# Performance work log

Measured on AMD Instinct MI355X. Metric: run time of the kernel, lower is better.

## Reference

```python
import jax, jax.numpy as jnp
import numpy as np

NEG_INF = -1e30  # stand-in for float('-inf') that is softmax-safe


def setup_inputs() -> dict:
    key = jax.random.key(0)
    ks = jax.random.split(key, 6)
    B, H, S, D = 2, 8, 1024, 64
    NF, K = 4, 3
    return {
        "query": jax.random.normal(ks[0], (B, H, S, D), dtype=jnp.float32),
        "keys": jax.random.normal(ks[1], (B, H, S, D), dtype=jnp.float32),
        "vals": jax.random.normal(ks[2], (B, H, S, D), dtype=jnp.float32),
        "mask": jnp.ones((B, 1, S, S), dtype=jnp.int32),
        "conv_w": jax.random.normal(ks[3], (NF, 1, K, K), dtype=jnp.float32) * (1.0 / K),
        "conv_b": jnp.zeros((NF,), dtype=jnp.float32),
        "lin_w": jax.random.normal(ks[4], (1, NF), dtype=jnp.float32) * 0.5,
        "lin_b": jnp.zeros((1,), dtype=jnp.float32),
    }


def reference(query, keys, vals, mask, conv_w, conv_b, lin_w, lin_b):
    B, H, S, D = query.shape
    NF = conv_w.shape[0]
    K = conv_w.shape[2]
    scale = jnp.asarray(D, query.dtype) ** 0.5

    # [B,H,S,S] raw dot-product scores
    dp = jnp.einsum("bhsd,bhtd->bhst", query, keys) / scale

    # conv2d over the score matrix: treat (B*H) as batch, 1 input channel
    x = dp.reshape(B * H, 1, S, S)
    conv = jax.lax.conv_general_dilated(
        x, conv_w,
        window_strides=(1, 1),
        padding=[(K // 2, K // 2), (K // 2, K // 2)],
        dimension_numbers=("NCHW", "OIHW", "NCHW"),
    ) + conv_b[None, :, None, None]
    conv = jax.nn.leaky_relu(conv, negative_slope=0.01)  # [B*H, NF, S, S]

    # per-pixel linear over the filter axis (Linear(num_filters, 1))
    conv = conv.reshape(B, H, NF, S, S)
    preattn = jnp.einsum("bhfst,f->bhst", conv, lin_w[0]) + lin_b[0]

    # masking + softmax (mask broadcasts over heads)
    preattn = jnp.where(mask == 0, jnp.asarray(NEG_INF, preattn.dtype), preattn)
    attn = jax.nn.softmax(preattn, axis=-1)

    # dropout is identity in eval mode
    return jnp.einsum("bhst,bhtd->bhsd", attn, vals)
```

## Files before the change

### kernel.cpp

```cpp
#include <hip/hip_runtime.h>
#include <math.h>

#define S_LEN 1024
#define D_DIM 64
#define NBH   16

typedef unsigned short ushort_t;
typedef __attribute__((ext_vector_type(8))) short short8;
typedef __attribute__((ext_vector_type(4))) short short4v;
typedef __attribute__((ext_vector_type(4))) float f32x4;
typedef __attribute__((ext_vector_type(2))) float f32x2;

__device__ __forceinline__ ushort_t rne_bf16(float x) {
    unsigned u = __float_as_uint(x);
    return (ushort_t)((u + 0x7FFFu + ((u >> 16) & 1u)) >> 16);
}
__device__ __forceinline__ void split1(float x, ushort_t& h, ushort_t& l) {
    h = rne_bf16(x);
    float hf = __uint_as_float((unsigned)h << 16);
    l = rne_bf16(x - hf);
}

__global__ __launch_bounds__(256) void prep(
    const float* __restrict__ k, const float* __restrict__ v,
    const int* __restrict__ mask,
    ushort_t* __restrict__ khi, ushort_t* __restrict__ klo,
    ushort_t* __restrict__ vhi, ushort_t* __restrict__ vlo,
    unsigned* __restrict__ mw)
{
    __shared__ float Ls[64][65];
    const int tid = threadIdx.x;
    const int bx = blockIdx.x;
    if (bx < 512) {
        const int gid  = bx * 256 + tid;
        const int bh   = gid >> 13;
        const int tile = (gid >> 7) & 63;
        const int ch   = (gid >> 6) & 1;
        const int lane = gid & 63;
        const int quad = lane >> 4, t15 = lane & 15;
        const float* src = k + ((size_t)bh * S_LEN + tile * 16 + t15) * D_DIM
                             + ch * 32 + quad * 8;
        float x[8];
        *(float4*)(x + 0) = *(const float4*)(src);
        *(float4*)(x + 4) = *(const float4*)(src + 4);
        short8 hv, lv;
        #pragma unroll
        for (int i = 0; i < 8; ++i) {
            ushort_t h, l;
            split1(x[i], h, l);
            hv[i] = (short)h; lv[i] = (short)l;
        }
        *(short8*)(khi + (size_t)gid * 8) = hv;
        *(short8*)(klo + (size_t)gid * 8) = lv;
    } else if (bx < 768) {
        const int bi = bx - 512;
        const int tt = bi & 15, bh = bi >> 4;
        const float* vb = v + ((size_t)bh * S_LEN + tt * 64) * D_DIM;
        #pragma unroll
        for (int p = 0; p < 4; ++p) {
            int idx = p * 1024 + tid * 4;
            int r = idx >> 6, c = idx & 63;
            float4 x = *(const float4*)(vb + r * 64 + c);
            Ls[r][c] = x.x; Ls[r][c+1] = x.y; Ls[r][c+2] = x.z; Ls[r][c+3] = x.w;
        }
        __syncthreads();
        const int d = tid >> 2, c0 = (tid & 3) * 16;
        ushort_t hi[16], lo[16];
        #pragma unroll
        for (int j = 0; j < 16; ++j) split1(Ls[c0 + j][d], hi[j], lo[j]);
        const int tb0 = tt * 8 + (c0 >> 3);
        const size_t o0 = (((size_t)bh * 128 + tb0) * 64 + d) * 8;
        const size_t o1 = (((size_t)bh * 128 + tb0 + 1) * 64 + d) * 8;
        *(short8*)(vhi + o0) = *(short8*)(hi);
        *(short8*)(vhi + o1) = *(short8*)(hi + 8);
        *(short8*)(vlo + o0) = *(short8*)(lo);
        *(short8*)(vlo + o1) = *(short8*)(lo + 8);
    } else {
        const int gid = (bx - 768) * 256 + tid;
        const int row = gid >> 5, wd = gid & 31;
        const int4* mp = (const int4*)(mask + (size_t)row * 1024 + wd * 32);
        unsigned bits = 0;
        #pragma unroll
        for (int p = 0; p < 8; ++p) {
            int4 qv = mp[p];
            bits |= (qv.x != 0 ? 1u : 0u) << (p * 4 + 0);
            bits |= (qv.y != 0 ? 1u : 0u) << (p * 4 + 1);
            bits |= (qv.z != 0 ? 1u : 0u) << (p * 4 + 2);
            bits |= (qv.w != 0 ? 1u : 0u) << (p * 4 + 3);
        }
        mw[(size_t)row * 32 + wd] = bits;
    }
}

__global__ __launch_bounds__(256) void qk_mfma(
    const float* __restrict__ q,
    const ushort_t* __restrict__ khi, const ushort_t* __restrict__ klo,
    float* __restrict__ dp)
{
    __shared__ float Ls[4][16][68];
    const int st = blockIdx.x, bh = blockIdx.y;
    const int s0 = st * 16;
    const int tid = threadIdx.x;
    const int wave = tid >> 6, lane = tid & 63;
    const int m = lane & 15, quad = lane >> 4;

    const float* qp = q + ((size_t)bh * S_LEN + s0 + m) * D_DIM + quad * 8;
    float qa[16];
    *(float4*)(qa + 0)  = *(const float4*)(qp + 0);
    *(float4*)(qa + 4)  = *(const float4*)(qp + 4);
    *(float4*)(qa + 8)  = *(const float4*)(qp + 32);
    *(float4*)(qa + 12) = *(const float4*)(qp + 36);
    short8 ahi0, alo0, ahi1, alo1;
    #pragma unroll
    for (int i = 0; i < 8; ++i) {
        ushort_t h, l;
        split1(qa[i], h, l);      ahi0[i] = (short)h; alo0[i] = (short)l;
        split1(qa[8 + i], h, l);  ahi1[i] = (short)h; alo1[i] = (short)l;
    }

    float* dpb = dp + ((size_t)bh * S_LEN + s0) * S_LEN;

    #pragma unroll
    for (int sub = 0; sub < 4; ++sub) {
        #pragma unroll
        for (int tt = 0; tt < 4; ++tt) {
            const int tile = wave * 16 + sub * 4 + tt;
            const size_t kb = (((size_t)bh * 64 + tile) * 128 + lane) * 8;
            short8 bhi0 = *(const short8*)(khi + kb);
            short8 blo0 = *(const short8*)(klo + kb);
            short8 bhi1 = *(const short8*)(khi + kb + 512);
            short8 blo1 = *(const short8*)(klo + kb + 512);
            f32x4 acc = {0.f, 0.f, 0.f, 0.f};
            acc = __builtin_amdgcn_mfma_f32_16x16x32_bf16(ahi0, bhi0, acc, 0, 0, 0);
            acc = __builtin_amdgcn_mfma_f32_16x16x32_bf16(ahi0, blo0, acc, 0, 0, 0);
            acc = __builtin_amdgcn_mfma_f32_16x16x32_bf16(alo0, bhi0, acc, 0, 0, 0);
            acc = __builtin_amdgcn_mfma_f32_16x16x32_bf16(ahi1, bhi1, acc, 0, 0, 0);
            acc = __builtin_amdgcn_mfma_f32_16x16x32_bf16(ahi1, blo1, acc, 0, 0, 0);
            acc = __builtin_amdgcn_mfma_f32_16x16x32_bf16(alo1, bhi1, acc, 0, 0, 0);
            #pragma unroll
            for (int r = 0; r < 4; ++r)
                Ls[wave][quad * 4 + r][tt * 16 + m] = acc[r] * 0.125f;
        }
        const int cb = wave * 256 + sub * 64;
        #pragma unroll
        for (int p = 0; p < 4; ++p) {
            const int row = p * 4 + (lane >> 4);
            const int f4  = lane & 15;
            float4 val = *(const float4*)&Ls[wave][row][f4 * 4];
            *(float4*)&dpb[(size_t)row * S_LEN + cb + f4 * 4] = val;
        }
    }
}

#define PSTR 1048
__global__ __launch_bounds__(512) void conv_av(
    const float* __restrict__ dp, const unsigned* __restrict__ mw,
    const ushort_t* __restrict__ vhi, const ushort_t* __restrict__ vlo,
    const float* __restrict__ conv_w, const float* __restrict__ conv_b,
    const float* __restrict__ lin_w, const float* __restrict__ lin_b,
    float* __restrict__ out)
{
    __shared__ ushort_t pP[16 * PSTR];
    __shared__ float oBuf[16][68];
    __shared__ float lsPart[16][4];
    __shared__ unsigned mb[16][32];

    const int st = blockIdx.x, bh = blockIdx.y;
    const int s0 = st * 16;
    const int b  = bh >> 3;
    const int tid = threadIdx.x;
    const int wave = tid >> 6, lane = tid & 63;
    const int m = lane & 15, quad = lane >> 4;

    {
        const int row = tid >> 5, wd = tid & 31;
        mb[row][wd] = mw[((size_t)b * S_LEN + s0 + row) * 32 + wd];
    }

    float w[36];
    #pragma unroll
    for (int i = 0; i < 36; ++i) w[i] = conv_w[i];
    float cb[4], lw[4];
    #pragma unroll
    for (int f = 0; f < 4; ++f) { cb[f] = conv_b[f]; lw[f] = lin_w[f]; }
    const float lb = lin_b[0];

    const int rh = tid >> 8, cg = tid & 255, c0 = cg * 4;
    const float* dpb = dp + (size_t)bh * S_LEN * S_LEN;
    __syncthreads();

    #pragma unroll
    for (int pass = 0; pass < 2; ++pass) {
        const int obase = rh * 8 + pass * 4;
        float rowv[6][6];
        #pragma unroll
        for (int jj = 0; jj < 6; ++jj) {
            const int ir = s0 + obase - 1 + jj;
            if (ir >= 0 && ir < S_LEN) {
                const float* rp = dpb + (size_t)ir * S_LEN + c0;
                f32x4 md = *(const f32x4*)rp;
                rowv[jj][0] = cg ? rp[-1] : 0.f;
                rowv[jj][1] = md.x; rowv[jj][2] = md.y;
                rowv[jj][3] = md.z; rowv[jj][4] = md.w;
                rowv[jj][5] = (cg < 255) ? rp[4] : 0.f;
            } else {
                #pragma unroll
                for (int i = 0; i < 6; ++i) rowv[jj][i] = 0.f;
            }
        }
        float ls[4];
        #pragma unroll
        for (int jo = 0; jo < 4; ++jo) {
            const int o = obase + jo;
            f32x2 pa = {lb, lb}, pb = {lb, lb};
            #pragma unroll
            for (int f = 0; f < 4; ++f) {
                f32x2 ca = {cb[f], cb[f]}, cbv = ca;
                #pragma unroll
                for (int dr = 0; dr < 3; ++dr) {
                    const float* vv = rowv[jo + dr];
                    #pragma unroll
                    for (int dc = 0; dc < 3; ++dc) {
                        const float wt = w[f * 9 + dr * 3 + dc];
                        f32x2 ia = {vv[dc],     vv[dc + 1]};
                        f32x2 ib = {vv[dc + 2], vv[dc + 3]};
                        ca  += wt * ia;
                        cbv += wt * ib;
                    }
                }
                f32x2 la  = {fmaxf(ca.x, 0.f)  + 0.01f * fminf(ca.x, 0.f),
                             fmaxf(ca.y, 0.f)  + 0.01f * fminf(ca.y, 0.f)};
                f32x2 lb2 = {fmaxf(cbv.x, 0.f) + 0.01f * fminf(cbv.x, 0.f),
                             fmaxf(cbv.y, 0.f) + 0.01f * fminf(cbv.y, 0.f)};
                pa += lw[f] * la;
                pb += lw[f] * lb2;
            }
            const unsigned word = mb[o][cg >> 3];
            const unsigned nib  = (word >> ((cg & 7) * 4)) & 0xFu;
            float pre[4] = {pa.x, pa.y, pb.x, pb.y};
            #pragma unroll
            for (int i = 0; i < 4; ++i)
                if (!((nib >> i) & 1u)) pre[i] = -1e30f;
            float pv[4];
            #pragma unroll
            for (int i = 0; i < 4; ++i) pv[i] = __expf(pre[i]);
            ls[jo] = (pv[0] + pv[1]) + (pv[2] + pv[3]);
            short4v hv = {(short)rne_bf16(pv[0]), (short)rne_bf16(pv[1]),
                          (short)rne_bf16(pv[2]), (short)rne_bf16(pv[3])};
            *(short4v*)&pP[o * PSTR + c0] = hv;
        }
        #pragma unroll
        for (int jo = 0; jo < 4; ++jo) {
            float t = ls[jo];
            #pragma unroll
            for (int off = 1; off < 64; off <<= 1) t += __shfl_xor(t, off);
            if (lane == 0) lsPart[obase + jo][wave & 3] = t;
        }
    }
    __syncthreads();

    const int d0 = (wave & 3) * 16;
    const int th = wave >> 2;
    f32x4 O = {0.f, 0.f, 0.f, 0.f};
    #pragma unroll 4
    for (int i = 0; i < 16; ++i) {
        const int c = th * 16 + i;
        short8 ph = *(const short8*)&pP[m * PSTR + c * 32 + quad * 8];
        const size_t vb = (((size_t)bh * 128 + c * 4 + quad) * 64 + d0 + m) * 8;
        short8 vh = *(const short8*)(vhi + vb);
        short8 vl = *(const short8*)(vlo + vb);
        O = __builtin_amdgcn_mfma_f32_16x16x32_bf16(ph, vh, O, 0, 0, 0);
        O = __builtin_amdgcn_mfma_f32_16x16x32_bf16(ph, vl, O, 0, 0, 0);
    }
    if (wave < 4) {
        #pragma unroll
        for (int r = 0; r < 4; ++r) oBuf[quad * 4 + r][d0 + m] = O[r];
    }
    __syncthreads();
    if (wave >= 4) {
        #pragma unroll
        for (int r = 0; r < 4; ++r) {
            const int br = quad * 4 + r;
            const float lsum = (lsPart[br][0] + lsPart[br][1]) +
                               (lsPart[br][2] + lsPart[br][3]);
            out[((size_t)bh * S_LEN + s0 + br) * D_DIM + d0 + m] =
                (O[r] + oBuf[br][d0 + m]) / lsum;
        }
    }
}

extern "C" void kernel_launch(void* const* d_in, const int* in_sizes, int n_in,
                              void* d_out, int out_size, void* d_ws, size_t ws_size,
                              hipStream_t stream) {
    const float* q      = (const float*)d_in[0];
    const float* k      = (const float*)d_in[1];
    const float* v      = (const float*)d_in[2];
    const int*   mask   = (const int*)d_in[3];
    const float* conv_w = (const float*)d_in[4];
    const float* conv_b = (const float*)d_in[5];
    const float* lin_w  = (const float*)d_in[6];
    const float* lin_b  = (const float*)d_in[7];
    float* out = (float*)d_out;

    char* wsb = (char*)d_ws;
    const size_t MB = 1024 * 1024;
    ushort_t* khi = (ushort_t*)(wsb + 0 * MB);
    ushort_t* klo = (ushort_t*)(wsb + 2 * MB);
    ushort_t* vhi = (ushort_t*)(wsb + 4 * MB);
    ushort_t* vlo = (ushort_t*)(wsb + 6 * MB);
    unsigned* mw  = (unsigned*)(wsb + 8 * MB);
    float*    dp  = (float*)(wsb + 16 * MB);

    prep<<<dim3(1024), 256, 0, stream>>>(k, v, mask, khi, klo, vhi, vlo, mw);
    qk_mfma<<<dim3(64, NBH), 256, 0, stream>>>(q, khi, klo, dp);
    conv_av<<<dim3(64, NBH), 512, 0, stream>>>(
        dp, mw, vhi, vlo, conv_w, conv_b, lin_w, lin_b, out);
}
```

Baseline: 136.2 us.

## Fuse QK score computation into conv/AV kernel with fp16 LDS halo tile

Removes the separate qk_mfma kernel and the 64 MB fp32 score matrix round-trip through global memory. Each block now computes its 16 score rows plus a one-row halo on each side directly with MFMA and stores them as fp16 in shared memory for the 3x3 conv stage. The cost is recomputing halo rows, extra MFMA work for the second 16-row set, more LDS per block (which may lower occupancy), and fp16 rounding of the scores before the conv.

Result: faster. 131.8 us (-3.2%).

```diff
diff --git a/kernel.cpp b/kernel.cpp
--- a/kernel.cpp
+++ b/kernel.cpp
@@ -6,10 +6,12 @@
 #define NBH   16
 
 typedef unsigned short ushort_t;
+typedef unsigned int uint_t;
 typedef __attribute__((ext_vector_type(8))) short short8;
 typedef __attribute__((ext_vector_type(4))) short short4v;
 typedef __attribute__((ext_vector_type(4))) float f32x4;
 typedef __attribute__((ext_vector_type(2))) float f32x2;
+typedef __attribute__((ext_vector_type(2))) _Float16 h2;
 
 __device__ __forceinline__ ushort_t rne_bf16(float x) {
     unsigned u = __float_as_uint(x);
@@ -19,6 +21,22 @@
     h = rne_bf16(x);
     float hf = __uint_as_float((unsigned)h << 16);
     l = rne_bf16(x - hf);
+}
+__device__ __forceinline__ ushort_t f16bits(float x) {
+    _Float16 h = (_Float16)x;
+    ushort_t b;
+    __builtin_memcpy(&b, &h, 2);
+    return b;
+}
+__device__ __forceinline__ float h2f(ushort_t b) {
+    _Float16 h;
+    __builtin_memcpy(&h, &b, 2);
+    return (float)h;
+}
+__device__ __forceinline__ h2 as_h2(uint_t u) {
+    h2 r;
+    __builtin_memcpy(&r, &u, 4);
+    return r;
 }
 
 __global__ __launch_bounds__(256) void prep(
@@ -92,74 +110,18 @@
     }
 }
 
-__global__ __launch_bounds__(256) void qk_mfma(
+#define DPSTR 1040
+#define PSTR  1048
+__global__ __launch_bounds__(512) void fused_qk_conv_av(
     const float* __restrict__ q,
     const ushort_t* __restrict__ khi, const ushort_t* __restrict__ klo,
-    float* __restrict__ dp)
-{
-    __shared__ float Ls[4][16][68];
-    const int st = blockIdx.x, bh = blockIdx.y;
-    const int s0 = st * 16;
-    const int tid = threadIdx.x;
-    const int wave = tid >> 6, lane = tid & 63;
-    const int m = lane & 15, quad = lane >> 4;
-
-    const float* qp = q + ((size_t)bh * S_LEN + s0 + m) * D_DIM + quad * 8;
-    float qa[16];
-    *(float4*)(qa + 0)  = *(const float4*)(qp + 0);
-    *(float4*)(qa + 4)  = *(const float4*)(qp + 4);
-    *(float4*)(qa + 8)  = *(const float4*)(qp + 32);
-    *(float4*)(qa + 12) = *(const float4*)(qp + 36);
-    short8 ahi0, alo0, ahi1, alo1;
-    #pragma unroll
-    for (int i = 0; i < 8; ++i) {
-        ushort_t h, l;
-        split1(qa[i], h, l);      ahi0[i] = (short)h; alo0[i] = (short)l;
-        split1(qa[8 + i], h, l);  ahi1[i] = (short)h; alo1[i] = (short)l;
-    }
-
-    float* dpb = dp + ((size_t)bh * S_LEN + s0) * S_LEN;
-
-    #pragma unroll
-    for (int sub = 0; sub < 4; ++sub) {
-        #pragma unroll
-        for (int tt = 0; tt < 4; ++tt) {
-            const int tile = wave * 16 + sub * 4 + tt;
-            const size_t kb = (((size_t)bh * 64 + tile) * 128 + lane) * 8;
-            short8 bhi0 = *(const short8*)(khi + kb);
-            short8 blo0 = *(const short8*)(klo + kb);
-            short8 bhi1 = *(const short8*)(khi + kb + 512);
-            short8 blo1 = *(const short8*)(klo + kb + 512);
-            f32x4 acc = {0.f, 0.f, 0.f, 0.f};
-            acc = __builtin_amdgcn_mfma_f32_16x16x32_bf16(ahi0, bhi0, acc, 0, 0, 0);
-            acc = __builtin_amdgcn_mfma_f32_16x16x32_bf16(ahi0, blo0, acc, 0, 0, 0);
-            acc = __builtin_amdgcn_mfma_f32_16x16x32_bf16(alo0, bhi0, acc, 0, 0, 0);
-            acc = __builtin_amdgcn_mfma_f32_16x16x32_bf16(ahi1, bhi1, acc, 0, 0, 0);
-            acc = __builtin_amdgcn_mfma_f32_16x16x32_bf16(ahi1, blo1, acc, 0, 0, 0);
-            acc = __builtin_amdgcn_mfma_f32_16x16x32_bf16(alo1, bhi1, acc, 0, 0, 0);
-            #pragma unroll
-            for (int r = 0; r < 4; ++r)
-                Ls[wave][quad * 4 + r][tt * 16 + m] = acc[r] * 0.125f;
-        }
-        const int cb = wave * 256 + sub * 64;
-        #pragma unroll
-        for (int p = 0; p < 4; ++p) {
-            const int row = p * 4 + (lane >> 4);
-            const int f4  = lane & 15;
-            float4 val = *(const float4*)&Ls[wave][row][f4 * 4];
-            *(float4*)&dpb[(size_t)row * S_LEN + cb + f4 * 4] = val;
-        }
-    }
-}
-
-#define PSTR 1048
-__global__ __launch_bounds__(512) void conv_av(
-    const float* __restrict__ dp, const unsigned* __restrict__ mw,
+    const unsigned* __restrict__ mw,
     const ushort_t* __restrict__ vhi, const ushort_t* __restrict__ vlo,
     const float* __restrict__ conv_w, const float* __restrict__ conv_b,
     const float* __restrict__ lin_w, const float* __restrict__ lin_b,
     float* __restrict__ out)
 {
+    __shared__ ushort_t dpH[18 * DPSTR];
     __shared__ ushort_t pP[16 * PSTR];
     __shared__ float oBuf[16][68];
     __shared__ float lsPart[16][4];
@@ -177,6 +139,72 @@
         mb[row][wd] = mw[((size_t)b * S_LEN + s0 + row) * 32 + wd];
     }
 
+    short8 AH0[2], AH1[2], AL0[2], AL1[2];
+    #pragma unroll
+    for (int set = 0; set < 2; ++set) {
+        const int sA = s0 - 1 + 2 * set + m;
+        const int sQ = sA < 0 ? 0 : (sA > S_LEN - 1 ? S_LEN - 1 : sA);
+        const float* qp = q + ((size_t)bh * S_LEN + sQ) * D_DIM + quad * 8;
+        float qa[16];
+        *(float4*)(qa + 0)  = *(const float4*)(qp + 0);
+        *(float4*)(qa + 4)  = *(const float4*)(qp + 4);
+        *(float4*)(qa + 8)  = *(const float4*)(qp + 32);
+        *(float4*)(qa + 12) = *(const float4*)(qp + 36);
+        #pragma unroll
+        for (int i = 0; i < 8; ++i) {
+            ushort_t h, l;
+            split1(qa[i] * 0.125f, h, l);
+            AH0[set][i] = (short)h; AL0[set][i] = (short)l;
+            split1(qa[8 + i] * 0.125f, h, l);
+            AH1[set][i] = (short)h; AL1[set][i] = (short)l;
+        }
+    }
+
+    #pragma unroll
+    for (int tt = 0; tt < 8; ++tt) {
+        const int tile = wave * 8 + tt;
+        const size_t kb = (((size_t)bh * 64 + tile) * 128 + lane) * 8;
+        short8 KH0 = *(const short8*)(khi + kb);
+        short8 KL0 = *(const short8*)(klo + kb);
+        short8 KH1 = *(const short8*)(khi + kb + 512);
+        short8 KL1 = *(const short8*)(klo + kb + 512);
+        const int col = tile * 16 + m;
+        {
+            f32x4 a0 = {0.f, 0.f, 0.f, 0.f}, a1 = {0.f, 0.f, 0.f, 0.f};
+            a0 = __builtin_amdgcn_mfma_f32_16x16x32_bf16(AH0[0], KH0, a0, 0, 0, 0);
+            a1 = __builtin_amdgcn_mfma_f32_16x16x32_bf16(AH1[0], KH1, a1, 0, 0, 0);
+            a0 = __builtin_amdgcn_mfma_f32_16x16x32_bf16(AH0[0], KL0, a0, 0, 0, 0);
+            a1 = __builtin_amdgcn_mfma_f32_16x16x32_bf16(AH1[0], KL1, a1, 0, 0, 0);
+            a0 = __builtin_amdgcn_mfma_f32_16x16x32_bf16(AL0[0], KH0, a0, 0, 0, 0);
+            a1 = __builtin_amdgcn_mfma_f32_16x16x32_bf16(AL1[0], KH1, a1, 0, 0, 0);
+            #pragma unroll
+            for (int r = 0; r < 4; ++r) {
+                const int row = quad * 4 + r;
+                const int s = s0 - 1 + row;
+                const float v = (s >= 0 && s < S_LEN) ? a0[r] + a1[r] : 0.f;
+                dpH[row * DPSTR + col] = f16bits(v);
+            }
+        }
+        {
+            f32x4 a0 = {0.f, 0.f, 0.f, 0.f}, a1 = {0.f, 0.f, 0.f, 0.f};
+            a0 = __builtin_amdgcn_mfma_f32_16x16x32_bf16(AH0[1], KH0, a0, 0, 0, 0);
+            a1 = __builtin_amdgcn_mfma_f32_16x16x32_bf16(AH1[1], KH1, a1, 0, 0, 0);
+            a0 = __builtin_amdgcn_mfma_f32_16x16x32_bf16(AH0[1], KL0, a0, 0, 0, 0);
+            a1 = __builtin_amdgcn_mfma_f32_16x16x32_bf16(AH1[1], KL1, a1, 0, 0, 0);
+            a0 = __builtin_amdgcn_mfma_f32_16x16x32_bf16(AL0[1], KH0, a0, 0, 0, 0);
+            a1 = __builtin_amdgcn_mfma_f32_16x16x32_bf16(AL1[1], KH1, a1, 0, 0, 0);
+            if (quad == 3) {
+                #pragma unroll
+                for (int r = 2; r < 4; ++r) {
+                    const int mrow = quad * 4 + r;
+                    const int s = s0 + 1 + mrow;
+                    const float v = (s < S_LEN) ? a0[r] + a1[r] : 0.f;
+                    dpH[(mrow + 2) * DPSTR + col] = f16bits(v);
+                }
+            }
+        }
+    }
+
     float w[36];
     #pragma unroll
     for (int i = 0; i < 36; ++i) w[i] = conv_w[i];
@@ -185,28 +213,22 @@
     for (int f = 0; f < 4; ++f) { cb[f] = conv_b[f]; lw[f] = lin_w[f]; }
     const float lb = lin_b[0];
 
+    __syncthreads();
+
     const int rh = tid >> 8, cg = tid & 255, c0 = cg * 4;
-    const float* dpb = dp + (size_t)bh * S_LEN * S_LEN;
-    __syncthreads();
-
     #pragma unroll
     for (int pass = 0; pass < 2; ++pass) {
         const int obase = rh * 8 + pass * 4;
         float rowv[6][6];
         #pragma unroll
         for (int jj = 0; jj < 6; ++jj) {
-            const int ir = s0 + obase - 1 + jj;
-            if (ir >= 0 && ir < S_LEN) {
-                const float* rp = dpb + (size_t)ir * S_LEN + c0;
-                f32x4 md = *(const f32x4*)rp;
-                rowv[jj][0] = cg ? rp[-1] : 0.f;
-                rowv[jj][1] = md.x; rowv[jj][2] = md.y;
-                rowv[jj][3] = md.z; rowv[jj][4] = md.w;
-                rowv[jj][5] = (cg < 255) ? rp[4] : 0.f;
-            } else {
-                #pragma unroll
-                for (int i = 0; i < 6; ++i) rowv[jj][i] = 0.f;
-            }
+            const ushort_t* rp = &dpH[(obase + jj) * DPSTR + c0];
+            uint2 dd = *(const uint2*)rp;
+            h2 p0 = as_h2(dd.x), p1 = as_h2(dd.y);
+            rowv[jj][0] = cg ? h2f(rp[-1]) : 0.f;
+            rowv[jj][1] = (float)p0[0]; rowv[jj][2] = (float)p0[1];
+            rowv[jj][3] = (float)p1[0]; rowv[jj][4] = (float)p1[1];
+            rowv[jj][5] = (cg < 255) ? h2f(rp[4]) : 0.f;
         }
         float ls[4];
         #pragma unroll
@@ -309,10 +331,8 @@
     ushort_t* vhi = (ushort_t*)(wsb + 4 * MB);
     ushort_t* vlo = (ushort_t*)(wsb + 6 * MB);
     unsigned* mw  = (unsigned*)(wsb + 8 * MB);
-    float*    dp  = (float*)(wsb + 16 * MB);
 
     prep<<<dim3(1024), 256, 0, stream>>>(k, v, mask, khi, klo, vhi, vlo, mw);
-    qk_mfma<<<dim3(64, NBH), 256, 0, stream>>>(q, khi, klo, dp);
-    conv_av<<<dim3(64, NBH), 512, 0, stream>>>(
-        dp, mw, vhi, vlo, conv_w, conv_b, lin_w, lin_b, out);
-}
+    fused_qk_conv_av<<<dim3(64, NBH), 512, 0, stream>>>(
+        q, khi, klo, mw, vhi, vlo, conv_w, conv_b, lin_w, lin_b, out);
+}
```
